# Performance work log

Measured on AMD Instinct MI355X. Metric: run time of the kernel, lower is better.

Reference implementation:

```python
import jax, jax.numpy as jnp
import numpy as np

N_HEADS = 8
N_DIM = 512
ATTN_DIM = N_DIM // N_HEADS
SOFT_TEMPERATURE = 1.0
TEMPERATURE = ATTN_DIM ** 0.5 / SOFT_TEMPERATURE


def sparsemax(z):
    # sparsemax along last axis: euclidean projection onto the simplex
    n = z.shape[-1]
    z_sorted = -jnp.sort(-z, axis=-1)                      # descending
    cs = jnp.cumsum(z_sorted, axis=-1)
    k = jnp.arange(1, n + 1, dtype=z.dtype)
    support = 1.0 + k * z_sorted > cs                      # bool
    k_sel = jnp.sum(support, axis=-1, keepdims=True)       # support size >= 1
    cs_sel = jnp.take_along_axis(cs, k_sel - 1, axis=-1)
    tau = (cs_sel - 1.0) / k_sel.astype(z.dtype)
    return jnp.maximum(z - tau, 0.0)


def setup_inputs() -> dict:
    key = jax.random.key(0)
    ks = jax.random.split(key, 9)
    bs, L, d = 8, 1024, N_DIM
    s = 1.0 / np.sqrt(d)
    return {
        "h_q": jax.random.normal(ks[0], (bs, L, d), jnp.float32),
        "h_k": jax.random.normal(ks[1], (bs, L, d), jnp.float32),
        "h_v": jax.random.normal(ks[2], (bs, L, d), jnp.float32),
        "Wq": jax.random.normal(ks[3], (d, d), jnp.float32) * s,
        "Wk": jax.random.normal(ks[4], (d, d), jnp.float32) * s,
        "Wv": jax.random.normal(ks[5], (d, d), jnp.float32) * s,
        "bv": jax.random.normal(ks[6], (d,), jnp.float32) * s,
        "Wf": jax.random.normal(ks[7], (d, d), jnp.float32) * s,
        "bf": jax.random.normal(ks[8], (d,), jnp.float32) * s,
    }


def reference(h_q, h_k, h_v, Wq, Wk, Wv, bv, Wf, bf):
    bs, Lq, _ = h_q.shape
    Lk = h_k.shape[1]
    H, D = N_HEADS, ATTN_DIM
    q = (h_q @ Wq.T).reshape(bs, Lq, H, D).transpose(0, 2, 1, 3)   # bhqd
    k = (h_k @ Wk.T).reshape(bs, Lk, H, D).transpose(0, 2, 1, 3)   # bhkd
    v = (h_v @ Wv.T + bv).reshape(bs, Lk, H, D).transpose(0, 2, 1, 3)
    alpha = jnp.einsum('bhqd,bhkd->bhqk', q / TEMPERATURE, k)
    alpha = sparsemax(alpha)
    res = jnp.einsum('bhqk,bhkd->bhqd', alpha, v)
    res = res.transpose(0, 2, 1, 3).reshape(bs, Lq, H * D)
    return res @ Wf.T + bf
```

## Files before the change

### kernel.cpp

```cpp
#include <hip/hip_runtime.h>
#include <hip/hip_bf16.h>
#include <cstdint>
#include <cstddef>

#define BS 8
#define SEQ 1024
#define DMODEL 512
#define NHEADS 8
#define DHEAD 64
#define QBLK 16
#define PPAD 1032

typedef float f32x4 __attribute__((ext_vector_type(4)));
typedef short bf16x8 __attribute__((ext_vector_type(8)));

static __device__ __forceinline__ unsigned short f2bf(float v) {
    __hip_bfloat16 hb = __float2bfloat16(v);
    return *reinterpret_cast<unsigned short*>(&hb);
}

struct CvtJob { const float* s; unsigned short* d; int n4; };

__global__ __launch_bounds__(256) void cvt_many(
    CvtJob j0, CvtJob j1, CvtJob j2, CvtJob j3, CvtJob j4, CvtJob j5, CvtJob j6)
{
    CvtJob j;
    switch (blockIdx.y) {
        case 0: j = j0; break; case 1: j = j1; break; case 2: j = j2; break;
        case 3: j = j3; break; case 4: j = j4; break; case 5: j = j5; break;
        default: j = j6; break;
    }
    for (int i = blockIdx.x * 256 + threadIdx.x; i < j.n4; i += gridDim.x * 256) {
        const float4 f = ((const float4*)j.s)[i];
        uint2 u;
        u.x = (unsigned)f2bf(f.x) | ((unsigned)f2bf(f.y) << 16);
        u.y = (unsigned)f2bf(f.z) | ((unsigned)f2bf(f.w) << 16);
        ((uint2*)j.d)[i] = u;
    }
}

struct GArgs { const unsigned short* A; const unsigned short* W;
               const float* bias; void* C; void* C2; float scale; int mode; };

__global__ __launch_bounds__(256) void gemm_mfma(GArgs g0, GArgs g1, GArgs g2) {
    __shared__ __align__(16) unsigned short As[64 * 64];
    __shared__ __align__(16) unsigned short Bs[128 * 64];

    const GArgs g = (blockIdx.z == 0) ? g0 : ((blockIdx.z == 1) ? g1 : g2);
    const int tid = threadIdx.x;
    const int w = tid >> 6, l = tid & 63, lr = l & 15, lg = l >> 4;
    const int bm = blockIdx.y * 64, bn = blockIdx.x * 128;
    const int mrow = (w & 1) * 32, ncol = (w >> 1) * 64;

    f32x4 acc[2][4];
#pragma unroll
    for (int mt = 0; mt < 2; ++mt)
#pragma unroll
        for (int nt = 0; nt < 4; ++nt) acc[mt][nt] = (f32x4)0.f;

    for (int k0 = 0; k0 < DMODEL; k0 += 64) {
#pragma unroll
        for (int i = 0; i < 2; ++i) {
            const int rbase = i * 32 + w * 8;
            const int r = rbase + (l >> 3);
            const unsigned short* src = g.A + (size_t)(bm + r) * DMODEL + k0
                                        + 8 * ((l & 7) ^ (r & 7));
            __builtin_amdgcn_global_load_lds((const unsigned int*)src,
                                             (unsigned int*)&As[rbase * 64], 16, 0, 0);
        }
#pragma unroll
        for (int i = 0; i < 4; ++i) {
            const int rbase = i * 32 + w * 8;
            const int r = rbase + (l >> 3);
            const unsigned short* src = g.W + (size_t)(bn + r) * DMODEL + k0
                                        + 8 * ((l & 7) ^ (r & 7));
            __builtin_amdgcn_global_load_lds((const unsigned int*)src,
                                             (unsigned int*)&Bs[rbase * 64], 16, 0, 0);
        }
        __syncthreads();
#pragma unroll
        for (int kk = 0; kk < 2; ++kk) {
            bf16x8 av[2], bv[4];
#pragma unroll
            for (int mt = 0; mt < 2; ++mt) {
                const int ra = mrow + mt * 16 + lr;
                av[mt] = *(const bf16x8*)&As[ra * 64 + 8 * ((kk * 4 + lg) ^ (ra & 7))];
            }
#pragma unroll
            for (int nt = 0; nt < 4; ++nt) {
                const int rb = ncol + nt * 16 + lr;
                bv[nt] = *(const bf16x8*)&Bs[rb * 64 + 8 * ((kk * 4 + lg) ^ (rb & 7))];
            }
#pragma unroll
            for (int mt = 0; mt < 2; ++mt)
#pragma unroll
                for (int nt = 0; nt < 4; ++nt)
                    acc[mt][nt] = __builtin_amdgcn_mfma_f32_16x16x32_bf16(
                        av[mt], bv[nt], acc[mt][nt], 0, 0, 0);
        }
        __syncthreads();
    }

    if (g.mode == 0) {
        float* C = (float*)g.C;
#pragma unroll
        for (int mt = 0; mt < 2; ++mt)
#pragma unroll
        for (int nt = 0; nt < 4; ++nt)
#pragma unroll
        for (int j = 0; j < 4; ++j) {
            const int r = bm + mrow + mt * 16 + lg * 4 + j;
            const int c = bn + ncol + nt * 16 + lr;
            C[(size_t)r * DMODEL + c] = acc[mt][nt][j] * g.scale
                                        + (g.bias ? g.bias[c] : 0.f);
        }
    } else {
        if (g.mode == 1 || g.mode == 3) {
            unsigned short* C = (unsigned short*)g.C;
#pragma unroll
            for (int mt = 0; mt < 2; ++mt)
#pragma unroll
            for (int nt = 0; nt < 4; ++nt)
#pragma unroll
            for (int j = 0; j < 4; ++j) {
                const int r = bm + mrow + mt * 16 + lg * 4 + j;
                const int c = bn + ncol + nt * 16 + lr;
                const float v = acc[mt][nt][j] * g.scale + (g.bias ? g.bias[c] : 0.f);
                const int b = r >> 10, ll = r & (SEQ - 1);
                const int h = c >> 6, dd = c & 63;
                C[((size_t)(b * NHEADS + h) * SEQ + ll) * DHEAD + dd] = f2bf(v);
            }
        }
        if (g.mode == 2 || g.mode == 3) {
            unsigned short* C = (unsigned short*)((g.mode == 3) ? g.C2 : g.C);
#pragma unroll
            for (int mt = 0; mt < 2; ++mt)
#pragma unroll
            for (int nt = 0; nt < 4; ++nt) {
                const int c = bn + ncol + nt * 16 + lr;
                const int h = c >> 6, dd = c & 63;
                const int r0 = bm + mrow + mt * 16 + lg * 4;
                const int b = r0 >> 10, l0 = r0 & (SEQ - 1);
                unsigned short tmp[4];
#pragma unroll
                for (int j = 0; j < 4; ++j)
                    tmp[j] = f2bf(acc[mt][nt][j] * g.scale + (g.bias ? g.bias[c] : 0.f));
                uint2 u;
                u.x = (unsigned)tmp[0] | ((unsigned)tmp[1] << 16);
                u.y = (unsigned)tmp[2] | ((unsigned)tmp[3] << 16);
                *(uint2*)&C[((size_t)(b * NHEADS + h) * DHEAD + dd) * SEQ + l0] = u;
            }
        }
    }
}

__global__ __launch_bounds__(256, 4) void attn_mfma(
    const unsigned short* __restrict__ Q, const unsigned short* __restrict__ K,
    const unsigned short* __restrict__ Vt, const unsigned short* __restrict__ Vn,
    unsigned short* __restrict__ R)
{
    __shared__ __align__(16) unsigned short P[QBLK][PPAD];
    __shared__ __align__(16) float clist[QBLK][66];
    __shared__ __align__(16) unsigned short cidx[QBLK][66];
    __shared__ int cnt_s[QBLK];
    __shared__ __align__(16) float red_m[QBLK][4];
    __shared__ __align__(16) float red_s[2][QBLK][4];
    __shared__ __align__(16) float red_c[2][QBLK][4];
    __shared__ float tau_s[QBLK];

    const int tid = threadIdx.x;
    const int w = tid >> 6, l = tid & 63, lr = l & 15, lg = l >> 4;

    const int flat = blockIdx.x;
    const int nid = (flat & 7) * 512 + (flat >> 3);
    const int q0 = (nid & 63) * QBLK;
    const int h = (nid >> 6) & (NHEADS - 1);
    const int b = nid >> 9;

    const size_t base = (size_t)(b * NHEADS + h) * SEQ * DHEAD;
    const unsigned short* Qp = Q + base;
    const unsigned short* Kp = K + base;

    const int ks = w * 256;

    const bf16x8 aq0 = *(const bf16x8*)(Qp + (size_t)(q0 + lr) * DHEAD + lg * 8);
    const bf16x8 aq1 = *(const bf16x8*)(Qp + (size_t)(q0 + lr) * DHEAD + 32 + lg * 8);
#define KROW(T) (Kp + (size_t)(ks + (T) * 16 + lr) * DHEAD + lg * 8)
    bf16x8 ka0 = *(const bf16x8*)KROW(0), kb0 = *(const bf16x8*)(KROW(0) + 32);
    bf16x8 ka1 = *(const bf16x8*)KROW(1), kb1 = *(const bf16x8*)(KROW(1) + 32);
    bf16x8 ka2 = *(const bf16x8*)KROW(2), kb2 = *(const bf16x8*)(KROW(2) + 32);
    bf16x8 ka3 = *(const bf16x8*)KROW(3), kb3 = *(const bf16x8*)(KROW(3) + 32);
    f32x4 acc[16];
#pragma unroll
    for (int t = 0; t < 16; ++t) acc[t] = (f32x4)0.f;
#define QK_STEP(T, KA, KB)                                                     \
    {                                                                          \
        acc[T] = __builtin_amdgcn_mfma_f32_16x16x32_bf16(KA, aq0, acc[T], 0, 0, 0); \
        acc[T] = __builtin_amdgcn_mfma_f32_16x16x32_bf16(KB, aq1, acc[T], 0, 0, 0); \
        if ((T) + 4 < 16) {                                                    \
            KA = *(const bf16x8*)KROW((T) + 4);                                \
            KB = *(const bf16x8*)(KROW((T) + 4) + 32);                         \
        }                                                                      \
    }
#pragma unroll
    for (int t = 0; t < 16; t += 4) {
        QK_STEP(t + 0, ka0, kb0)
        QK_STEP(t + 1, ka1, kb1)
        QK_STEP(t + 2, ka2, kb2)
        QK_STEP(t + 3, ka3, kb3)
    }
#undef QK_STEP
#undef KROW

    f32x4 m4 = acc[0];
#pragma unroll
    for (int t = 1; t < 16; ++t) {
        m4[0] = fmaxf(m4[0], acc[t][0]); m4[1] = fmaxf(m4[1], acc[t][1]);
        m4[2] = fmaxf(m4[2], acc[t][2]); m4[3] = fmaxf(m4[3], acc[t][3]);
    }
    float m = fmaxf(fmaxf(m4[0], m4[1]), fmaxf(m4[2], m4[3]));
    m = fmaxf(m, __shfl_xor(m, 16));
    m = fmaxf(m, __shfl_xor(m, 32));
    if (lg == 0) red_m[lr][w] = m;

    for (int i = tid; i < QBLK * 66; i += 256) (&clist[0][0])[i] = -3.0e38f;
    if (tid < QBLK) cnt_s[tid] = 0;
    __syncthreads();

    const float4 rm4 = *(const float4*)red_m[lr];
    const float rmax = fmaxf(fmaxf(rm4.x, rm4.y), fmaxf(rm4.z, rm4.w));
    float tau = rmax - 1.0f;
    const float thr = tau;

#pragma unroll
    for (int t = 0; t < 16; ++t)
#pragma unroll
        for (int j = 0; j < 4; ++j) {
            const float z = acc[t][j];
            if (z > thr) {
                const int pos = atomicAdd(&cnt_s[lr], 1);
                if (pos < 64) {
                    clist[lr][pos] = z;
                    cidx[lr][pos] = (unsigned short)(ks + t * 16 + lg * 4 + j);
                }
            }
        }
    __syncthreads();

    const bool anyfull = __any(cnt_s[lr] > 64);

    if (!anyfull) {
        const f32x4* clp = (const f32x4*)&clist[lr][lg * 16];
        const f32x4 cd0 = clp[0], cd1 = clp[1], cd2 = clp[2], cd3 = clp[3];
        for (int it = 0; it < 16; ++it) {
            float s = 0.f, c = 0.f;
#pragma unroll
            for (int i = 0; i < 4; ++i) {
                const float z0 = cd0[i], z1 = cd1[i], z2 = cd2[i], z3 = cd3[i];
                if (z0 > tau) { s += z0; c += 1.f; }
                if (z1 > tau) { s += z1; c += 1.f; }
                if (z2 > tau) { s += z2; c += 1.f; }
                if (z3 > tau) { s += z3; c += 1.f; }
            }
            s += __shfl_xor(s, 16); c += __shfl_xor(c, 16);
            s += __shfl_xor(s, 32); c += __shfl_xor(c, 32);
            const float tn = (s - 1.f) / c;
            float delta = tn - tau;
            tau = tn;
            delta = fmaxf(delta, __shfl_xor(delta, 1));
            delta = fmaxf(delta, __shfl_xor(delta, 2));
            delta = fmaxf(delta, __shfl_xor(delta, 4));
            delta = fmaxf(delta, __shfl_xor(delta, 8));
            if (delta < 1e-5f) break;
        }
        if (w == 0 && lg == 0) tau_s[lr] = tau;
        __syncthreads();

        const int r = tid >> 4;
        const int dt = tid & 15;
        const float taur = tau_s[r];
        const int cntc = cnt_s[r];
        const unsigned short* Vrow = Vn + base + dt * 4;
        f32x4 o = (f32x4)0.f;
        float z0, z1, z2, z3;
        uint2 v0, v1, v2, v3;
#define SLOAD(ZS, VS, I)                                                       \
    {                                                                          \
        const int ii = (I) < cntc ? (I) : 0;                                   \
        ZS = clist[r][ii];                                                     \
        VS = *(const uint2*)(Vrow + (size_t)cidx[r][ii] * DHEAD);              \
    }
#define SMAC(ZS, VS)                                                           \
    {                                                                          \
        const float wgt = fmaxf(ZS - taur, 0.f);                               \
        o[0] += wgt * __uint_as_float(VS.x << 16);                             \
        o[1] += wgt * __uint_as_float(VS.x & 0xffff0000u);                     \
        o[2] += wgt * __uint_as_float(VS.y << 16);                             \
        o[3] += wgt * __uint_as_float(VS.y & 0xffff0000u);                     \
    }
        SLOAD(z0, v0, 0) SLOAD(z1, v1, 1) SLOAD(z2, v2, 2) SLOAD(z3, v3, 3)
        for (int i = 0; i < cntc; i += 4) {
            SMAC(z0, v0)
            if (i + 1 < cntc) SMAC(z1, v1)
            if (i + 2 < cntc) SMAC(z2, v2)
            if (i + 3 < cntc) SMAC(z3, v3)
            SLOAD(z0, v0, i + 4) SLOAD(z1, v1, i + 5)
            SLOAD(z2, v2, i + 6) SLOAD(z3, v3, i + 7)
        }
#undef SLOAD
#undef SMAC
        unsigned short t4[4];
#pragma unroll
        for (int j = 0; j < 4; ++j) t4[j] = f2bf(o[j]);
        uint2 u;
        u.x = (unsigned)t4[0] | ((unsigned)t4[1] << 16);
        u.y = (unsigned)t4[2] | ((unsigned)t4[3] << 16);
        *(uint2*)&R[((size_t)b * SEQ + q0 + r) * DMODEL + h * DHEAD + dt * 4] = u;
        return;
    }

    for (int it = 0; it < 16; ++it) {
        const int bb = (it + 1) & 1;
        float s = 0.f, c = 0.f;
#pragma unroll
        for (int t = 0; t < 16; ++t)
#pragma unroll
            for (int j = 0; j < 4; ++j) {
                const float z = acc[t][j];
                if (z > tau) { s += z; c += 1.f; }
            }
        s += __shfl_xor(s, 16); c += __shfl_xor(c, 16);
        s += __shfl_xor(s, 32); c += __shfl_xor(c, 32);
        if (lg == 0) { red_s[bb][lr][w] = s; red_c[bb][lr][w] = c; }
        __syncthreads();
        const float4 s4 = *(const float4*)red_s[bb][lr];
        const float4 c4 = *(const float4*)red_c[bb][lr];
        const float st = (s4.x + s4.y) + (s4.z + s4.w);
        const float ct = (c4.x + c4.y) + (c4.z + c4.w);
        const float tn = (st - 1.f) / ct;
        float delta = tn - tau;
        tau = tn;
        delta = fmaxf(delta, __shfl_xor(delta, 1));
        delta = fmaxf(delta, __shfl_xor(delta, 2));
        delta = fmaxf(delta, __shfl_xor(delta, 4));
        delta = fmaxf(delta, __shfl_xor(delta, 8));
        if (delta < 1e-5f) break;
    }

#pragma unroll
    for (int t = 0; t < 16; ++t)
#pragma unroll
        for (int jp = 0; jp < 2; ++jp) {
            const unsigned lo = f2bf(fmaxf(acc[t][2 * jp] - tau, 0.f));
            const unsigned hi = f2bf(fmaxf(acc[t][2 * jp + 1] - tau, 0.f));
            *(unsigned*)&P[lr][ks + t * 16 + lg * 4 + 2 * jp] = lo | (hi << 16);
        }
    __syncthreads();

    const int dcol = w * 16;
    const unsigned short* VtP = Vt + ((size_t)(b * NHEADS + h) * DHEAD + dcol + lr) * SEQ
                                + lg * 8;
    f32x4 o = (f32x4)0.f;
    bf16x8 vb0 = *(const bf16x8*)(VtP + 0 * 32);
    bf16x8 vb1 = *(const bf16x8*)(VtP + 1 * 32);
    bf16x8 vb2 = *(const bf16x8*)(VtP + 2 * 32);
    bf16x8 vb3 = *(const bf16x8*)(VtP + 3 * 32);
#define PV_STEP(KT, VREG)                                                      \
    {                                                                          \
        const bf16x8 pa = *(const bf16x8*)&P[lr][(KT) * 32 + lg * 8];          \
        o = __builtin_amdgcn_mfma_f32_16x16x32_bf16(pa, VREG, o, 0, 0, 0);     \
        if ((KT) + 4 < 32) VREG = *(const bf16x8*)(VtP + ((KT) + 4) * 32);     \
    }
    for (int kt = 0; kt < 32; kt += 4) {
        PV_STEP(kt + 0, vb0)
        PV_STEP(kt + 1, vb1)
        PV_STEP(kt + 2, vb2)
        PV_STEP(kt + 3, vb3)
    }
#undef PV_STEP

#pragma unroll
    for (int j = 0; j < 4; ++j)
        R[((size_t)b * SEQ + q0 + lg * 4 + j) * DMODEL + h * DHEAD + dcol + lr] =
            f2bf(o[j]);
}

extern "C" void kernel_launch(void* const* d_in, const int* in_sizes, int n_in,
                              void* d_out, int out_size, void* d_ws, size_t ws_size,
                              hipStream_t stream) {
    const float* h_q = (const float*)d_in[0];
    const float* h_k = (const float*)d_in[1];
    const float* h_v = (const float*)d_in[2];
    const float* Wq  = (const float*)d_in[3];
    const float* Wk  = (const float*)d_in[4];
    const float* Wv  = (const float*)d_in[5];
    const float* bv  = (const float*)d_in[6];
    const float* Wf  = (const float*)d_in[7];
    const float* bf  = (const float*)d_in[8];
    float* out = (float*)d_out;

    const size_t perT = (size_t)BS * SEQ * DMODEL;
    const size_t wN = (size_t)DMODEL * DMODEL;
    unsigned short* hq_b = (unsigned short*)d_ws;
    unsigned short* hk_b = hq_b + perT;
    unsigned short* hv_b = hk_b + perT;
    unsigned short* Qws  = hv_b + perT;
    unsigned short* Kws  = Qws + perT;
    unsigned short* Vtw  = Kws + perT;
    unsigned short* Vnw  = Vtw + perT;
    unsigned short* Rws  = Vnw + perT;
    unsigned short* Wqb  = Rws + perT;
    unsigned short* Wkb  = Wqb + wN;
    unsigned short* Wvb  = Wkb + wN;
    unsigned short* Wfb  = Wvb + wN;

    {
        CvtJob j0{h_q, hq_b, (int)(perT / 4)};
        CvtJob j1{h_k, hk_b, (int)(perT / 4)};
        CvtJob j2{h_v, hv_b, (int)(perT / 4)};
        CvtJob j3{Wq, Wqb, (int)(wN / 4)};
        CvtJob j4{Wk, Wkb, (int)(wN / 4)};
        CvtJob j5{Wv, Wvb, (int)(wN / 4)};
        CvtJob j6{Wf, Wfb, (int)(wN / 4)};
        cvt_many<<<dim3(512, 7), 256, 0, stream>>>(j0, j1, j2, j3, j4, j5, j6);
    }

    {
        GArgs gq{hq_b, Wqb, nullptr, Qws, nullptr, 0.125f, 1};
        GArgs gk{hk_b, Wkb, nullptr, Kws, nullptr, 1.0f, 1};
        GArgs gv{hv_b, Wvb, bv,      Vnw, Vtw,     1.0f, 3};
        gemm_mfma<<<dim3(DMODEL / 128, BS * SEQ / 64, 3), 256, 0, stream>>>(gq, gk, gv);
    }

    attn_mfma<<<dim3(BS * NHEADS * (SEQ / QBLK)), 256, 0, stream>>>(Qws, Kws, Vtw, Vnw, Rws);

    {
        GArgs gf{Rws, Wfb, bf, out, nullptr, 1.0f, 0};
        gemm_mfma<<<dim3(DMODEL / 128, BS * SEQ / 64, 1), 256, 0, stream>>>(gf, gf, gf);
    }
}
```

Baseline: 190.6 us.

## Split attention into QK candidate-extraction kernel and sparse finalize kernel

Splits the fused attention kernel into two launches. The first computes QK scores and writes a capped per-row candidate list (CAP=56) to a global scratch buffer. The second loads those candidates, solves for the sparsemax threshold using a per-row 16-lane reduction, and does the sparse PV accumulation, recomputing the dense path only on overflow. The aim is lighter kernels with less shared memory and fewer registers and barriers, which should raise occupancy. The cost is an extra launch and a round trip through global memory, and overflow rows now recompute QK.

Result: slower. 244.2 us (+28.1%).

```diff
diff --git a/kernel.cpp b/kernel.cpp
--- a/kernel.cpp
+++ b/kernel.cpp
@@ -10,6 +10,8 @@
 #define DHEAD 64
 #define QBLK 16
 #define PPAD 1032
+#define CAP 56
+#define TILE_BYTES (16*CAP*4 + 16*CAP*2 + 16*2)
 
 typedef float f32x4 __attribute__((ext_vector_type(4)));
 typedef short bf16x8 __attribute__((ext_vector_type(8)));
@@ -154,19 +156,14 @@
     }
 }
 
-__global__ __launch_bounds__(256, 4) void attn_mfma(
+__global__ __launch_bounds__(256) void attn_qk(
     const unsigned short* __restrict__ Q, const unsigned short* __restrict__ K,
-    const unsigned short* __restrict__ Vt, const unsigned short* __restrict__ Vn,
-    unsigned short* __restrict__ R)
+    unsigned char* __restrict__ cand)
 {
-    __shared__ __align__(16) unsigned short P[QBLK][PPAD];
-    __shared__ __align__(16) float clist[QBLK][66];
-    __shared__ __align__(16) unsigned short cidx[QBLK][66];
+    __shared__ float clv[16 * CAP];
+    __shared__ unsigned short cli[16 * CAP];
     __shared__ int cnt_s[QBLK];
     __shared__ __align__(16) float red_m[QBLK][4];
-    __shared__ __align__(16) float red_s[2][QBLK][4];
-    __shared__ __align__(16) float red_c[2][QBLK][4];
-    __shared__ float tau_s[QBLK];
 
     const int tid = threadIdx.x;
     const int w = tid >> 6, l = tid & 63, lr = l & 15, lg = l >> 4;
@@ -180,7 +177,6 @@
     const size_t base = (size_t)(b * NHEADS + h) * SEQ * DHEAD;
     const unsigned short* Qp = Q + base;
     const unsigned short* Kp = K + base;
-
     const int ks = w * 256;
 
     const bf16x8 aq0 = *(const bf16x8*)(Qp + (size_t)(q0 + lr) * DHEAD + lg * 8);
@@ -223,14 +219,14 @@
     m = fmaxf(m, __shfl_xor(m, 32));
     if (lg == 0) red_m[lr][w] = m;
 
-    for (int i = tid; i < QBLK * 66; i += 256) (&clist[0][0])[i] = -3.0e38f;
+    for (int i = tid; i < 16 * CAP; i += 256) clv[i] = -3.0e38f;
+    for (int i = tid; i < 16 * CAP; i += 256) cli[i] = 0;
     if (tid < QBLK) cnt_s[tid] = 0;
     __syncthreads();
 
     const float4 rm4 = *(const float4*)red_m[lr];
     const float rmax = fmaxf(fmaxf(rm4.x, rm4.y), fmaxf(rm4.z, rm4.w));
-    float tau = rmax - 1.0f;
-    const float thr = tau;
+    const float thr = rmax - 1.0f;
 
 #pragma unroll
     for (int t = 0; t < 16; ++t)
@@ -239,46 +235,88 @@
             const float z = acc[t][j];
             if (z > thr) {
                 const int pos = atomicAdd(&cnt_s[lr], 1);
-                if (pos < 64) {
-                    clist[lr][pos] = z;
-                    cidx[lr][pos] = (unsigned short)(ks + t * 16 + lg * 4 + j);
+                if (pos < CAP) {
+                    clv[lr * CAP + pos] = z;
+                    cli[lr * CAP + pos] = (unsigned short)(ks + t * 16 + lg * 4 + j);
                 }
             }
         }
     __syncthreads();
 
-    const bool anyfull = __any(cnt_s[lr] > 64);
+    unsigned char* tp = cand + (size_t)nid * TILE_BYTES;
+    float* gv = (float*)tp;
+    unsigned short* gi = (unsigned short*)(tp + 16 * CAP * 4);
+    unsigned short* gc = (unsigned short*)(tp + 16 * CAP * 6);
+    for (int i = tid; i < 16 * CAP; i += 256) gv[i] = clv[i];
+    for (int i = tid; i < 16 * CAP; i += 256) gi[i] = cli[i];
+    if (tid < 16) gc[tid] = (unsigned short)(cnt_s[tid] > 1023 ? 1023 : cnt_s[tid]);
+}
+
+__global__ __launch_bounds__(256) void attn_fin(
+    const unsigned short* __restrict__ Q, const unsigned short* __restrict__ K,
+    const unsigned short* __restrict__ Vt, const unsigned short* __restrict__ Vn,
+    const unsigned char* __restrict__ cand, unsigned short* __restrict__ R)
+{
+    __shared__ float svals[16 * CAP];
+    __shared__ unsigned short sidx[16 * CAP];
+    __shared__ int cnt_s[QBLK];
+    __shared__ __align__(16) unsigned short P[QBLK][PPAD];
+    __shared__ __align__(16) float red_m[QBLK][4];
+    __shared__ __align__(16) float red_s[2][QBLK][4];
+    __shared__ __align__(16) float red_c[2][QBLK][4];
+
+    const int tid = threadIdx.x;
+    const int nid = blockIdx.x;
+    const int q0 = (nid & 63) * QBLK;
+    const int h = (nid >> 6) & (NHEADS - 1);
+    const int b = nid >> 9;
+    const size_t base = (size_t)(b * NHEADS + h) * SEQ * DHEAD;
+
+    const unsigned char* tp = cand + (size_t)nid * TILE_BYTES;
+    const float* gv = (const float*)tp;
+    const unsigned short* gi = (const unsigned short*)(tp + 16 * CAP * 4);
+    const unsigned short* gc = (const unsigned short*)(tp + 16 * CAP * 6);
+    for (int i = tid; i < 16 * CAP; i += 256) svals[i] = gv[i];
+    for (int i = tid; i < 16 * CAP; i += 256) sidx[i] = gi[i];
+    if (tid < 16) cnt_s[tid] = gc[tid];
+    __syncthreads();
+
+    const int l = tid & 63;
+    const bool anyfull = __any(cnt_s[l & 15] > CAP);
 
     if (!anyfull) {
-        const f32x4* clp = (const f32x4*)&clist[lr][lg * 16];
-        const f32x4 cd0 = clp[0], cd1 = clp[1], cd2 = clp[2], cd3 = clp[3];
+        const int r = tid >> 4;
+        const int dt = tid & 15;
+        float z[4];
+#pragma unroll
+        for (int k = 0; k < 4; ++k) {
+            const int s = dt * 4 + k;
+            z[k] = (s < CAP) ? svals[r * CAP + s] : -3.0e38f;
+        }
+        float m = fmaxf(fmaxf(z[0], z[1]), fmaxf(z[2], z[3]));
+        m = fmaxf(m, __shfl_xor(m, 1));
+        m = fmaxf(m, __shfl_xor(m, 2));
+        m = fmaxf(m, __shfl_xor(m, 4));
+        m = fmaxf(m, __shfl_xor(m, 8));
+        float tau = m - 1.0f;
         for (int it = 0; it < 16; ++it) {
             float s = 0.f, c = 0.f;
 #pragma unroll
-            for (int i = 0; i < 4; ++i) {
-                const float z0 = cd0[i], z1 = cd1[i], z2 = cd2[i], z3 = cd3[i];
-                if (z0 > tau) { s += z0; c += 1.f; }
-                if (z1 > tau) { s += z1; c += 1.f; }
-                if (z2 > tau) { s += z2; c += 1.f; }
-                if (z3 > tau) { s += z3; c += 1.f; }
-            }
-            s += __shfl_xor(s, 16); c += __shfl_xor(c, 16);
-            s += __shfl_xor(s, 32); c += __shfl_xor(c, 32);
+            for (int k = 0; k < 4; ++k)
+                if (z[k] > tau) { s += z[k]; c += 1.f; }
+            s += __shfl_xor(s, 1); c += __shfl_xor(c, 1);
+            s += __shfl_xor(s, 2); c += __shfl_xor(c, 2);
+            s += __shfl_xor(s, 4); c += __shfl_xor(c, 4);
+            s += __shfl_xor(s, 8); c += __shfl_xor(c, 8);
             const float tn = (s - 1.f) / c;
             float delta = tn - tau;
             tau = tn;
-            delta = fmaxf(delta, __shfl_xor(delta, 1));
-            delta = fmaxf(delta, __shfl_xor(delta, 2));
-            delta = fmaxf(delta, __shfl_xor(delta, 4));
-            delta = fmaxf(delta, __shfl_xor(delta, 8));
+            delta = fmaxf(delta, __shfl_xor(delta, 16));
+            delta = fmaxf(delta, __shfl_xor(delta, 32));
             if (delta < 1e-5f) break;
         }
-        if (w == 0 && lg == 0) tau_s[lr] = tau;
-        __syncthreads();
-
-        const int r = tid >> 4;
-        const int dt = tid & 15;
-        const float taur = tau_s[r];
+
+        const float taur = tau;
         const int cntc = cnt_s[r];
         const unsigned short* Vrow = Vn + base + dt * 4;
         f32x4 o = (f32x4)0.f;
@@ -287,8 +325,8 @@
 #define SLOAD(ZS, VS, I)                                                       \
     {                                                                          \
         const int ii = (I) < cntc ? (I) : 0;                                   \
-        ZS = clist[r][ii];                                                     \
-        VS = *(const uint2*)(Vrow + (size_t)cidx[r][ii] * DHEAD);              \
+        ZS = svals[r * CAP + ii];                                              \
+        VS = *(const uint2*)(Vrow + (size_t)sidx[r * CAP + ii] * DHEAD);       \
     }
 #define SMAC(ZS, VS)                                                           \
     {                                                                          \
@@ -319,70 +357,103 @@
         return;
     }
 
-    for (int it = 0; it < 16; ++it) {
-        const int bb = (it + 1) & 1;
-        float s = 0.f, c = 0.f;
+    {
+        const int w = tid >> 6, lr = l & 15, lg = l >> 4;
+        const unsigned short* Qp = Q + base;
+        const unsigned short* Kp = K + base;
+        const int ks = w * 256;
+        const bf16x8 aq0 = *(const bf16x8*)(Qp + (size_t)(q0 + lr) * DHEAD + lg * 8);
+        const bf16x8 aq1 = *(const bf16x8*)(Qp + (size_t)(q0 + lr) * DHEAD + 32 + lg * 8);
+        f32x4 acc[16];
+#pragma unroll
+        for (int t = 0; t < 16; ++t) acc[t] = (f32x4)0.f;
+#pragma unroll
+        for (int t = 0; t < 16; ++t) {
+            const unsigned short* kp = Kp + (size_t)(ks + t * 16 + lr) * DHEAD + lg * 8;
+            const bf16x8 bk0 = *(const bf16x8*)(kp);
+            const bf16x8 bk1 = *(const bf16x8*)(kp + 32);
+            acc[t] = __builtin_amdgcn_mfma_f32_16x16x32_bf16(bk0, aq0, acc[t], 0, 0, 0);
+            acc[t] = __builtin_amdgcn_mfma_f32_16x16x32_bf16(bk1, aq1, acc[t], 0, 0, 0);
+        }
+        f32x4 m4 = acc[0];
+#pragma unroll
+        for (int t = 1; t < 16; ++t) {
+            m4[0] = fmaxf(m4[0], acc[t][0]); m4[1] = fmaxf(m4[1], acc[t][1]);
+            m4[2] = fmaxf(m4[2], acc[t][2]); m4[3] = fmaxf(m4[3], acc[t][3]);
+        }
+        float m = fmaxf(fmaxf(m4[0], m4[1]), fmaxf(m4[2], m4[3]));
+        m = fmaxf(m, __shfl_xor(m, 16));
+        m = fmaxf(m, __shfl_xor(m, 32));
+        if (lg == 0) red_m[lr][w] = m;
+        __syncthreads();
+        const float4 rm4 = *(const float4*)red_m[lr];
+        float tau = fmaxf(fmaxf(rm4.x, rm4.y), fmaxf(rm4.z, rm4.w)) - 1.0f;
+
+        for (int it = 0; it < 16; ++it) {
+            const int bb = (it + 1) & 1;
+            float s = 0.f, c = 0.f;
+#pragma unroll
+            for (int t = 0; t < 16; ++t)
+#pragma unroll
+                for (int j = 0; j < 4; ++j) {
+                    const float z = acc[t][j];
+                    if (z > tau) { s += z; c += 1.f; }
+                }
+            s += __shfl_xor(s, 16); c += __shfl_xor(c, 16);
+            s += __shfl_xor(s, 32); c += __shfl_xor(c, 32);
+            if (lg == 0) { red_s[bb][lr][w] = s; red_c[bb][lr][w] = c; }
+            __syncthreads();
+            const float4 s4 = *(const float4*)red_s[bb][lr];
+            const float4 c4 = *(const float4*)red_c[bb][lr];
+            const float st = (s4.x + s4.y) + (s4.z + s4.w);
+            const float ct = (c4.x + c4.y) + (c4.z + c4.w);
+            const float tn = (st - 1.f) / ct;
+            float delta = tn - tau;
+            tau = tn;
+            delta = fmaxf(delta, __shfl_xor(delta, 1));
+            delta = fmaxf(delta, __shfl_xor(delta, 2));
+            delta = fmaxf(delta, __shfl_xor(delta, 4));
+            delta = fmaxf(delta, __shfl_xor(delta, 8));
+            if (delta < 1e-5f) break;
+        }
+
 #pragma unroll
         for (int t = 0; t < 16; ++t)
 #pragma unroll
-            for (int j = 0; j < 4; ++j) {
-                const float z = acc[t][j];
-                if (z > tau) { s += z; c += 1.f; }
+            for (int jp = 0; jp < 2; ++jp) {
+                const unsigned lo = f2bf(fmaxf(acc[t][2 * jp] - tau, 0.f));
+                const unsigned hi = f2bf(fmaxf(acc[t][2 * jp + 1] - tau, 0.f));
+                *(unsigned*)&P[lr][ks + t * 16 + lg * 4 + 2 * jp] = lo | (hi << 16);
             }
-        s += __shfl_xor(s, 16); c += __shfl_xor(c, 16);
-        s += __shfl_xor(s, 32); c += __shfl_xor(c, 32);
-        if (lg == 0) { red_s[bb][lr][w] = s; red_c[bb][lr][w] = c; }
         __syncthreads();
-        const float4 s4 = *(const float4*)red_s[bb][lr];
-        const float4 c4 = *(const float4*)red_c[bb][lr];
-        const float st = (s4.x + s4.y) + (s4.z + s4.w);
-        const float ct = (c4.x + c4.y) + (c4.z + c4.w);
-        const float tn = (st - 1.f) / ct;
-        float delta = tn - tau;
-        tau = tn;
-        delta = fmaxf(delta, __shfl_xor(delta, 1));
-        delta = fmaxf(delta, __shfl_xor(delta, 2));
-        delta = fmaxf(delta, __shfl_xor(delta, 4));
-        delta = fmaxf(delta, __shfl_xor(delta, 8));
-        if (delta < 1e-5f) break;
-    }
-
-#pragma unroll
-    for (int t = 0; t < 16; ++t)
-#pragma unroll
-        for (int jp = 0; jp < 2; ++jp) {
-            const unsigned lo = f2bf(fmaxf(acc[t][2 * jp] - tau, 0.f));
-            const unsigned hi = f2bf(fmaxf(acc[t][2 * jp + 1] - tau, 0.f));
-            *(unsigned*)&P[lr][ks + t * 16 + lg * 4 + 2 * jp] = lo | (hi << 16);
-        }
-    __syncthreads();
-
-    const int dcol = w * 16;
-    const unsigned short* VtP = Vt + ((size_t)(b * NHEADS + h) * DHEAD + dcol + lr) * SEQ
-                                + lg * 8;
-    f32x4 o = (f32x4)0.f;
-    bf16x8 vb0 = *(const bf16x8*)(VtP + 0 * 32);
-    bf16x8 vb1 = *(const bf16x8*)(VtP + 1 * 32);
-    bf16x8 vb2 = *(const bf16x8*)(VtP + 2 * 32);
-    bf16x8 vb3 = *(const bf16x8*)(VtP + 3 * 32);
+
+        const int dcol = w * 16;
+        const unsigned short* VtP = Vt + ((size_t)(b * NHEADS + h) * DHEAD + dcol + lr) * SEQ
+                                    + lg * 8;
+        f32x4 o = (f32x4)0.f;
+        bf16x8 vb0 = *(const bf16x8*)(VtP + 0 * 32);
+        bf16x8 vb1 = *(const bf16x8*)(VtP + 1 * 32);
+        bf16x8 vb2 = *(const bf16x8*)(VtP + 2 * 32);
+        bf16x8 vb3 = *(const bf16x8*)(VtP + 3 * 32);
 #define PV_STEP(KT, VREG)                                                      \
     {                                                                          \
         const bf16x8 pa = *(const bf16x8*)&P[lr][(KT) * 32 + lg * 8];          \
         o = __builtin_amdgcn_mfma_f32_16x16x32_bf16(pa, VREG, o, 0, 0, 0);     \
         if ((KT) + 4 < 32) VREG = *(const bf16x8*)(VtP + ((KT) + 4) * 32);     \
     }
-    for (int kt = 0; kt < 32; kt += 4) {
-        PV_STEP(kt + 0, vb0)
-        PV_STEP(kt + 1, vb1)
-        PV_STEP(kt + 2, vb2)
-        PV_STEP(kt + 3, vb3)
-    }
+        for (int kt = 0; kt < 32; kt += 4) {
+            PV_STEP(kt + 0, vb0)
+            PV_STEP(kt + 1, vb1)
+            PV_STEP(kt + 2, vb2)
+            PV_STEP(kt + 3, vb3)
+        }
 #undef PV_STEP
 
 #pragma unroll
-    for (int j = 0; j < 4; ++j)
-        R[((size_t)b * SEQ + q0 + lg * 4 + j) * DMODEL + h * DHEAD + dcol + lr] =
-            f2bf(o[j]);
+        for (int j = 0; j < 4; ++j)
+            R[((size_t)b * SEQ + q0 + lg * 4 + j) * DMODEL + h * DHEAD + dcol + lr] =
+                f2bf(o[j]);
+    }
 }
 
 extern "C" void kernel_launch(void* const* d_in, const int* in_sizes, int n_in,
@@ -413,6 +484,7 @@
     unsigned short* Wkb  = Wqb + wN;
     unsigned short* Wvb  = Wkb + wN;
     unsigned short* Wfb  = Wvb + wN;
+    unsigned char* cand = (unsigned char*)hq_b;
 
     {
         CvtJob j0{h_q, hq_b, (int)(perT / 4)};
@@ -432,7 +504,9 @@
         gemm_mfma<<<dim3(DMODEL / 128, BS * SEQ / 64, 3), 256, 0, stream>>>(gq, gk, gv);
     }
 
-    attn_mfma<<<dim3(BS * NHEADS * (SEQ / QBLK)), 256, 0, stream>>>(Qws, Kws, Vtw, Vnw, Rws);
+    attn_qk<<<dim3(BS * NHEADS * (SEQ / QBLK)), 256, 0, stream>>>(Qws, Kws, cand);
+    attn_fin<<<dim3(BS * NHEADS * (SEQ / QBLK)), 256, 0, stream>>>(Qws, Kws, Vtw, Vnw,
+                                                                   cand, Rws);
 
     {
         GArgs gf{Rws, Wfb, bf, out, nullptr, 1.0f, 0};
```

## Stage K tiles into LDS via async global_load_lds with double buffering

Applied to the files above, without the earlier changes.

Replaces per-wave direct global loads of K rows into registers with cooperative, double-buffered staging of 128-row K chunks into shared memory using global_load_lds, with an XOR swizzle to avoid bank conflicts. The LDS pool is aliased with the P buffer, and the key-to-wave mapping becomes interleaved across chunks, so the index math is updated. Occupancy hint drops from 4 to 3 blocks per CU to fit the larger LDS footprint. It adds a barrier per chunk and lowers occupancy in exchange for coalesced, asynchronous K loads.

After: 169.9 us. -10.8%, faster.

```diff
diff --git a/kernel.cpp b/kernel.cpp
--- a/kernel.cpp
+++ b/kernel.cpp
@@ -154,12 +154,12 @@
     }
 }
 
-__global__ __launch_bounds__(256, 4) void attn_mfma(
+__global__ __launch_bounds__(256, 3) void attn_mfma(
     const unsigned short* __restrict__ Q, const unsigned short* __restrict__ K,
     const unsigned short* __restrict__ Vt, const unsigned short* __restrict__ Vn,
     unsigned short* __restrict__ R)
 {
-    __shared__ __align__(16) unsigned short P[QBLK][PPAD];
+    __shared__ __align__(16) unsigned char pool[33024];
     __shared__ __align__(16) float clist[QBLK][66];
     __shared__ __align__(16) unsigned short cidx[QBLK][66];
     __shared__ int cnt_s[QBLK];
@@ -168,6 +168,9 @@
     __shared__ __align__(16) float red_c[2][QBLK][4];
     __shared__ float tau_s[QBLK];
 
+    unsigned short* Ks = (unsigned short*)pool;
+    unsigned short (*P)[PPAD] = (unsigned short (*)[PPAD])pool;
+
     const int tid = threadIdx.x;
     const int w = tid >> 6, l = tid & 63, lr = l & 15, lg = l >> 4;
 
@@ -181,42 +184,52 @@
     const unsigned short* Qp = Q + base;
     const unsigned short* Kp = K + base;
 
-    const int ks = w * 256;
-
     const bf16x8 aq0 = *(const bf16x8*)(Qp + (size_t)(q0 + lr) * DHEAD + lg * 8);
     const bf16x8 aq1 = *(const bf16x8*)(Qp + (size_t)(q0 + lr) * DHEAD + 32 + lg * 8);
-#define KROW(T) (Kp + (size_t)(ks + (T) * 16 + lr) * DHEAD + lg * 8)
-    bf16x8 ka0 = *(const bf16x8*)KROW(0), kb0 = *(const bf16x8*)(KROW(0) + 32);
-    bf16x8 ka1 = *(const bf16x8*)KROW(1), kb1 = *(const bf16x8*)(KROW(1) + 32);
-    bf16x8 ka2 = *(const bf16x8*)KROW(2), kb2 = *(const bf16x8*)(KROW(2) + 32);
-    bf16x8 ka3 = *(const bf16x8*)KROW(3), kb3 = *(const bf16x8*)(KROW(3) + 32);
+
+#define STAGE(CH, BUF)                                                         \
+    {                                                                          \
+        _Pragma("unroll")                                                      \
+        for (int i = 0; i < 4; ++i) {                                          \
+            const int rbase = i * 32 + w * 8;                                  \
+            const int r = rbase + (l >> 3);                                    \
+            const unsigned short* src = Kp + (size_t)((CH) * 128 + r) * DHEAD  \
+                                        + 8 * ((l & 7) ^ (r & 7));             \
+            __builtin_amdgcn_global_load_lds((const unsigned int*)src,         \
+                (unsigned int*)&Ks[(BUF) * 8192 + rbase * 64], 16, 0, 0);      \
+        }                                                                      \
+    }
+
     f32x4 acc[16];
 #pragma unroll
-    for (int t = 0; t < 16; ++t) acc[t] = (f32x4)0.f;
-#define QK_STEP(T, KA, KB)                                                     \
-    {                                                                          \
-        acc[T] = __builtin_amdgcn_mfma_f32_16x16x32_bf16(KA, aq0, acc[T], 0, 0, 0); \
-        acc[T] = __builtin_amdgcn_mfma_f32_16x16x32_bf16(KB, aq1, acc[T], 0, 0, 0); \
-        if ((T) + 4 < 16) {                                                    \
-            KA = *(const bf16x8*)KROW((T) + 4);                                \
-            KB = *(const bf16x8*)(KROW((T) + 4) + 32);                         \
-        }                                                                      \
-    }
-#pragma unroll
-    for (int t = 0; t < 16; t += 4) {
-        QK_STEP(t + 0, ka0, kb0)
-        QK_STEP(t + 1, ka1, kb1)
-        QK_STEP(t + 2, ka2, kb2)
-        QK_STEP(t + 3, ka3, kb3)
-    }
-#undef QK_STEP
-#undef KROW
+    for (int a = 0; a < 16; ++a) acc[a] = (f32x4)0.f;
+
+    STAGE(0, 0)
+    __syncthreads();
+#pragma unroll
+    for (int c = 0; c < 8; ++c) {
+        const int buf = c & 1;
+        if (c + 1 < 8) STAGE(c + 1, buf ^ 1)
+        const unsigned short* kb = Ks + buf * 8192;
+#pragma unroll
+        for (int tt = 0; tt < 2; ++tt) {
+            const int ra = w * 32 + tt * 16 + lr;
+            const bf16x8 k0 = *(const bf16x8*)&kb[ra * 64 + 8 * ((0 + lg) ^ (ra & 7))];
+            const bf16x8 k1 = *(const bf16x8*)&kb[ra * 64 + 8 * ((4 + lg) ^ (ra & 7))];
+            acc[2 * c + tt] = __builtin_amdgcn_mfma_f32_16x16x32_bf16(
+                k0, aq0, acc[2 * c + tt], 0, 0, 0);
+            acc[2 * c + tt] = __builtin_amdgcn_mfma_f32_16x16x32_bf16(
+                k1, aq1, acc[2 * c + tt], 0, 0, 0);
+        }
+        __syncthreads();
+    }
+#undef STAGE
 
     f32x4 m4 = acc[0];
 #pragma unroll
-    for (int t = 1; t < 16; ++t) {
-        m4[0] = fmaxf(m4[0], acc[t][0]); m4[1] = fmaxf(m4[1], acc[t][1]);
-        m4[2] = fmaxf(m4[2], acc[t][2]); m4[3] = fmaxf(m4[3], acc[t][3]);
+    for (int a = 1; a < 16; ++a) {
+        m4[0] = fmaxf(m4[0], acc[a][0]); m4[1] = fmaxf(m4[1], acc[a][1]);
+        m4[2] = fmaxf(m4[2], acc[a][2]); m4[3] = fmaxf(m4[3], acc[a][3]);
     }
     float m = fmaxf(fmaxf(m4[0], m4[1]), fmaxf(m4[2], m4[3]));
     m = fmaxf(m, __shfl_xor(m, 16));
@@ -233,15 +246,16 @@
     const float thr = tau;
 
 #pragma unroll
-    for (int t = 0; t < 16; ++t)
+    for (int a = 0; a < 16; ++a)
 #pragma unroll
         for (int j = 0; j < 4; ++j) {
-            const float z = acc[t][j];
+            const float z = acc[a][j];
             if (z > thr) {
                 const int pos = atomicAdd(&cnt_s[lr], 1);
                 if (pos < 64) {
                     clist[lr][pos] = z;
-                    cidx[lr][pos] = (unsigned short)(ks + t * 16 + lg * 4 + j);
+                    cidx[lr][pos] = (unsigned short)((a >> 1) * 128 + w * 32
+                                                     + (a & 1) * 16 + lg * 4 + j);
                 }
             }
         }
@@ -323,10 +337,10 @@
         const int bb = (it + 1) & 1;
         float s = 0.f, c = 0.f;
 #pragma unroll
-        for (int t = 0; t < 16; ++t)
+        for (int a = 0; a < 16; ++a)
 #pragma unroll
             for (int j = 0; j < 4; ++j) {
-                const float z = acc[t][j];
+                const float z = acc[a][j];
                 if (z > tau) { s += z; c += 1.f; }
             }
         s += __shfl_xor(s, 16); c += __shfl_xor(c, 16);
@@ -346,14 +360,16 @@
         delta = fmaxf(delta, __shfl_xor(delta, 8));
         if (delta < 1e-5f) break;
     }
-
-#pragma unroll
-    for (int t = 0; t < 16; ++t)
+    __syncthreads();
+
+#pragma unroll
+    for (int a = 0; a < 16; ++a)
 #pragma unroll
         for (int jp = 0; jp < 2; ++jp) {
-            const unsigned lo = f2bf(fmaxf(acc[t][2 * jp] - tau, 0.f));
-            const unsigned hi = f2bf(fmaxf(acc[t][2 * jp + 1] - tau, 0.f));
-            *(unsigned*)&P[lr][ks + t * 16 + lg * 4 + 2 * jp] = lo | (hi << 16);
+            const unsigned lo = f2bf(fmaxf(acc[a][2 * jp] - tau, 0.f));
+            const unsigned hi = f2bf(fmaxf(acc[a][2 * jp + 1] - tau, 0.f));
+            const int key = (a >> 1) * 128 + w * 32 + (a & 1) * 16 + lg * 4 + 2 * jp;
+            *(unsigned*)&P[lr][key] = lo | (hi << 16);
         }
     __syncthreads();
 
```
